# Kernel tuning notes

Measured on AMD Instinct MI355X. Metric: run time of the kernel, lower is better.

The kernel has to match this reference:

```python
import jax, jax.numpy as jnp
import numpy as np
import math

NUM_HEADS = 16
HEAD_SIZE = 64
SEQ_LEN = 2048
D_MODEL = NUM_HEADS * HEAD_SIZE
BATCH = 2


def _xavier(key, shape):
    fan_in, fan_out = shape[0], shape[1]
    limit = math.sqrt(6.0 / (fan_in + fan_out))
    return jax.random.uniform(key, shape, jnp.float32, -limit, limit)


def setup_inputs() -> dict:
    key = jax.random.key(0)
    ks = jax.random.split(key, 5)
    x = jax.random.normal(ks[0], (BATCH, SEQ_LEN, D_MODEL), jnp.float32)
    W_Q = _xavier(ks[1], (D_MODEL, D_MODEL))
    W_K = _xavier(ks[2], (D_MODEL, D_MODEL))
    W_V = _xavier(ks[3], (D_MODEL, D_MODEL))
    W_O = _xavier(ks[4], (D_MODEL, D_MODEL))
    zeros = jnp.zeros((D_MODEL,), jnp.float32)
    return {
        "x": x,
        "W_Q": W_Q, "W_K": W_K, "W_V": W_V, "W_O": W_O,
        "b_Q": zeros, "b_K": zeros, "b_V": zeros, "b_O": zeros,
    }


def _split_heads(t):
    # [B, S, H*d] -> [B, H, S, d]
    B, S, _ = t.shape
    return t.reshape(B, S, NUM_HEADS, HEAD_SIZE).transpose(0, 2, 1, 3)


def reference(x, W_Q, W_K, W_V, W_O, b_Q, b_K, b_V, b_O):
    q = _split_heads(x @ W_Q + b_Q)  # [B,H,S,d]
    k = _split_heads(x @ W_K + b_K)
    v = _split_heads(x @ W_V + b_V)

    # scores: [B,H,S,S]
    scores = jnp.einsum("bhqd,bhkd->bhqk", q, k)
    # Faithful to original: multiply by lower-triangular 0/1 mask, scale,
    # then add -10000 on strictly-upper positions (NOT -inf).
    tril = jnp.tril(jnp.ones((SEQ_LEN, SEQ_LEN), jnp.float32))
    neg_bias = jnp.triu(jnp.full((SEQ_LEN, SEQ_LEN), -10000.0, jnp.float32), 1)
    masked = scores * tril / np.sqrt(HEAD_SIZE).astype(np.float32) + neg_bias
    weights = jax.nn.softmax(masked, axis=-1)

    hs = jnp.einsum("bhqk,bhkd->bhqd", weights, v)  # [B,H,S,d]
    B = hs.shape[0]
    merged = hs.transpose(0, 2, 1, 3).reshape(B, SEQ_LEN, D_MODEL)
    return merged @ W_O + b_O
```

## Files before the change

### kernel.cpp

```cpp
#include <hip/hip_runtime.h>
#include <hip/hip_bf16.h>

#define S_LEN 2048
#define NH 16
#define HD 64
#define DM 1024
#define BATCH 2
#define M_ROWS (BATCH * S_LEN)
#define SCALE2 0.18033688011112043f
#define M2FIX 8.0f

typedef float f32x4 __attribute__((ext_vector_type(4)));
typedef __bf16 bf16x8 __attribute__((ext_vector_type(8)));
typedef short short8 __attribute__((ext_vector_type(8)));

__device__ __forceinline__ unsigned short f2bf(float f) {
  unsigned u = __builtin_bit_cast(unsigned, f);
  u += 0x7FFFu + ((u >> 16) & 1u);
  return (unsigned short)(u >> 16);
}

__device__ __forceinline__ f32x4 mfma16(bf16x8 a, bf16x8 b, f32x4 c) {
  return __builtin_amdgcn_mfma_f32_16x16x32_bf16(a, b, c, 0, 0, 0);
}

__device__ __forceinline__ void gload_lds16(const void* g, void* l) {
  __builtin_amdgcn_global_load_lds(
      (const __attribute__((address_space(1))) void*)g,
      (__attribute__((address_space(3))) void*)l, 16, 0, 0);
}

__global__ __launch_bounds__(256) void cast_bf16_kernel(
    const float* __restrict__ in, unsigned short* __restrict__ out) {
  int i = blockIdx.x * 256 + threadIdx.x;
  const float4* p = (const float4*)in;
  float4 f0 = p[i * 2], f1 = p[i * 2 + 1];
  short8 o;
  o[0] = (short)f2bf(f0.x); o[1] = (short)f2bf(f0.y);
  o[2] = (short)f2bf(f0.z); o[3] = (short)f2bf(f0.w);
  o[4] = (short)f2bf(f1.x); o[5] = (short)f2bf(f1.y);
  o[6] = (short)f2bf(f1.z); o[7] = (short)f2bf(f1.w);
  ((short8*)out)[i] = o;
}

__global__ __launch_bounds__(256) void transpose_cast_kernel(
    const float* __restrict__ W0, const float* __restrict__ W1,
    const float* __restrict__ W2, const float* __restrict__ W3,
    unsigned short* __restrict__ out) {
  int z = blockIdx.z;
  const float* W = (z == 0) ? W0 : (z == 1) ? W1 : (z == 2) ? W2 : W3;
  __shared__ float tile[32][33];
  int tx = threadIdx.x & 31, ty = threadIdx.x >> 5;
  int bx = blockIdx.x * 32, by = blockIdx.y * 32;
#pragma unroll
  for (int i = 0; i < 4; ++i)
    tile[ty + i * 8][tx] = W[(size_t)(by + ty + i * 8) * DM + bx + tx];
  __syncthreads();
  unsigned short* o = out + (size_t)z * DM * DM;
#pragma unroll
  for (int i = 0; i < 4; ++i)
    o[(size_t)(bx + ty + i * 8) * DM + by + tx] = f2bf(tile[tx][ty + i * 8]);
}

template <int MODE>
__global__ __launch_bounds__(256) void gemm_bt_kernel(
    const unsigned short* __restrict__ A, const unsigned short* __restrict__ Bt,
    void* __restrict__ Cptr, const float* __restrict__ bias0,
    const float* __restrict__ bias1, const float* __restrict__ bias2,
    int M, int N, int K) {
  __shared__ __align__(16) unsigned short Sbuf[2][3][4096];
  unsigned short (*As)[4096] = Sbuf[0];
  unsigned short (*Bs)[4096] = Sbuf[1];
  const int t = threadIdx.x, lane = t & 63;
  const int wid = t >> 6, wr = wid >> 1, wc = wid & 1;
  const int r16 = lane & 15, g = lane >> 4;
  const int m0 = blockIdx.y * 128, n0 = blockIdx.x * 128;
  const int nk = K >> 5;

  const int n1 = t, n2 = t + 256;
  const int r1g = t >> 2, c1g = (t & 3) * 8;
  const int r2g = (t + 256) >> 2;

  const unsigned short* ap1 = A + (size_t)(m0 + r1g) * K + c1g;
  const unsigned short* ap2 = A + (size_t)(m0 + r2g) * K + c1g;
  const unsigned short* bp1 = Bt + (size_t)(n0 + r1g) * K + c1g;
  const unsigned short* bp2 = Bt + (size_t)(n0 + r2g) * K + c1g;

#define GSTAGE(s)                          \
  gload_lds16(ap1, &As[s][n1 * 8]);        \
  gload_lds16(bp1, &Bs[s][n1 * 8]);        \
  gload_lds16(ap2, &As[s][n2 * 8]);        \
  gload_lds16(bp2, &Bs[s][n2 * 8]);        \
  ap1 += 32; ap2 += 32; bp1 += 32; bp2 += 32;

  f32x4 acc[4][4] = {};

  GSTAGE(0);
  GSTAGE(1);

  for (int kt = 0; kt < nk; ++kt) {
    const int cs = kt % 3;
    if (kt + 1 < nk) {
      asm volatile("s_waitcnt vmcnt(4)" ::: "memory");
    } else {
      asm volatile("s_waitcnt vmcnt(0)" ::: "memory");
    }
    __builtin_amdgcn_s_barrier();
    if (kt + 2 < nk) { GSTAGE((kt + 2) % 3); }

    bf16x8 af[4], bfr[4];
#pragma unroll
    for (int mi = 0; mi < 4; ++mi)
      af[mi] = *(const bf16x8*)&As[cs][(wr * 64 + mi * 16 + r16) * 32 + g * 8];
#pragma unroll
    for (int ni = 0; ni < 4; ++ni)
      bfr[ni] = *(const bf16x8*)&Bs[cs][(wc * 64 + ni * 16 + r16) * 32 + g * 8];
    __builtin_amdgcn_s_setprio(1);
#pragma unroll
    for (int mi = 0; mi < 4; ++mi)
#pragma unroll
      for (int ni = 0; ni < 4; ++ni)
        acc[mi][ni] = mfma16(af[mi], bfr[ni], acc[mi][ni]);
    __builtin_amdgcn_s_setprio(0);
  }
#undef GSTAGE

  if (MODE == 0) {
    unsigned short* Cb = (unsigned short*)Cptr;
    const int buf = n0 >> 10;
    if (buf < 2) {
      const float* bp = buf ? bias1 : bias0;
      const float sc = buf ? 1.0f : SCALE2;
#pragma unroll
      for (int ni = 0; ni < 4; ++ni) {
        int cn = (n0 & 1023) + wc * 64 + ni * 16 + r16;
        float bv = bp[cn];
#pragma unroll
        for (int mi = 0; mi < 4; ++mi) {
          int rowb = m0 + wr * 64 + mi * 16 + 4 * g;
#pragma unroll
          for (int j = 0; j < 4; ++j)
            Cb[(size_t)buf * 4194304u + (size_t)(rowb + j) * 1024 + cn] =
                __builtin_bit_cast(unsigned short, (__bf16)((acc[mi][ni][j] + bv) * sc));
        }
      }
    } else {
      unsigned short* T = &Sbuf[0][0][0];
      __syncthreads();
#pragma unroll
      for (int ni = 0; ni < 4; ++ni) {
        int cnl = wc * 64 + ni * 16 + r16;
        float bv = bias2[(n0 & 1023) + cnl];
#pragma unroll
        for (int mi = 0; mi < 4; ++mi) {
          int sl = wr * 64 + mi * 16 + 4 * g;
          union { __bf16 h4[4]; uint2 u; } cv;
#pragma unroll
          for (int j = 0; j < 4; ++j) cv.h4[j] = (__bf16)(acc[mi][ni][j] + bv);
          *(uint2*)&T[cnl * 136 + sl] = cv.u;
        }
      }
      __syncthreads();
      const int bb = m0 >> 11, s0g = m0 & 2047;
      unsigned short* Vt = Cb + 8388608u;
#pragma unroll
      for (int p = 0; p < 8; ++p) {
        int idx = p * 256 + t;
        int cnl = idx >> 4, sch = idx & 15;
        int cng = (n0 & 1023) + cnl;
        int hh = cng >> 6, d = cng & 63;
        short8 v = *(const short8*)&T[cnl * 136 + sch * 8];
        *(short8*)&Vt[(((size_t)((bb * 16 + hh) * 64 + d)) << 11) + s0g + sch * 8] = v;
      }
    }
  } else {
    float* Cf = (float*)Cptr;
#pragma unroll
    for (int ni = 0; ni < 4; ++ni) {
      int col = n0 + wc * 64 + ni * 16 + r16;
      float bv = bias0[col];
#pragma unroll
      for (int mi = 0; mi < 4; ++mi) {
        int rowb = m0 + wr * 64 + mi * 16 + 4 * g;
#pragma unroll
        for (int j = 0; j < 4; ++j)
          Cf[(size_t)(rowb + j) * N + col] = acc[mi][ni][j] + bv;
      }
    }
  }
}

__global__ __launch_bounds__(256) void attn_kernel(
    const unsigned short* __restrict__ Qm, const unsigned short* __restrict__ Km,
    const unsigned short* __restrict__ VtG, unsigned short* __restrict__ Om) {
  const int t = threadIdx.x, lane = t & 63, w = t >> 6;
  const int r16 = lane & 15, g = lane >> 4;
  const int bid = blockIdx.x;
  const int xk = bid & 7, slot = bid >> 3;
  const int grp = xk + 8 * (slot >> 4);
  const int mq = slot & 15;
  const int h = grp & 15, b = grp >> 4;

  __shared__ __align__(16) unsigned short Ks[2][8192];
  __shared__ __align__(16) unsigned short Vs[2][8192];
  __shared__ __align__(16) unsigned short Pl[4608];

  const unsigned short* Kbase = Km + (size_t)(b * S_LEN) * DM + h * HD;
  const unsigned short* Vbase = VtG + (size_t)((b * NH + h) * HD) * S_LEN;

  const int kc = ((t & 7) ^ ((t >> 3) & 7)) * 8;
  const int vc = ((t & 15) ^ (t >> 4)) * 8;
  const unsigned short* kp = Kbase + (size_t)(t >> 3) * DM + kc;
  const unsigned short* vp = Vbase + (size_t)(t >> 4) * S_LEN + vc;
  const int sxk = r16 & 7;
  const int qloc = w * 16 + r16;

  unsigned short* Pw = &Pl[w * 1152];
  unsigned* Pw32 = (unsigned*)Pw;

#define STAGE(s, kv0)                                                          \
  do {                                                                         \
    _Pragma("unroll") for (int p = 0; p < 4; ++p)                              \
        gload_lds16(kp + (size_t)((kv0) + 32 * p) * DM, &Ks[s][(t + 256 * p) * 8]); \
    _Pragma("unroll") for (int p = 0; p < 4; ++p)                              \
        gload_lds16(vp + (size_t)(16 * p) * S_LEN + (kv0), &Vs[s][(t + 256 * p) * 8]); \
  } while (0)

  for (int half = 0; half < 2; ++half) {
    const int qt = half ? 31 - mq : mq;
    const int q0 = qt * 64;
    const unsigned short* Qp = Qm + (size_t)(b * S_LEN + q0 + qloc) * DM + h * HD;
    bf16x8 qf0 = *(const bf16x8*)(Qp + g * 8);
    bf16x8 qf1 = *(const bf16x8*)(Qp + 32 + g * 8);

    f32x4 oacc[4] = {};
    float lsum = 0.f;
    const int nt2 = (qt + 2) >> 1;

    __syncthreads();
    STAGE(0, 0);

    for (int kt = 0; kt < nt2; ++kt) {
      const int cs = kt & 1;
      asm volatile("s_waitcnt vmcnt(0)" ::: "memory");
      __builtin_amdgcn_s_barrier();
      if (kt + 1 < nt2) { STAGE(cs ^ 1, (kt + 1) * 128); }

      const int kvbase = kt * 128;
#pragma unroll
      for (int u = 0; u < 2; ++u) {
        const int kvs = kvbase + u * 64;
        if (kvs > q0 + 63) break;

        f32x4 st[4];
#pragma unroll
        for (int ni = 0; ni < 4; ++ni) {
          int row = u * 64 + ni * 16 + r16;
          f32x4 z = {};
          bf16x8 kf0 = *(const bf16x8*)&Ks[cs][row * 64 + ((g ^ sxk) * 8)];
          bf16x8 kf1 = *(const bf16x8*)&Ks[cs][row * 64 + (((4 + g) ^ sxk) * 8)];
          __builtin_amdgcn_s_setprio(1);
          st[ni] = mfma16(kf1, qf1, mfma16(kf0, qf0, z));
          __builtin_amdgcn_s_setprio(0);
        }

        float p[4][4];
#pragma unroll
        for (int ni = 0; ni < 4; ++ni)
#pragma unroll
          for (int j = 0; j < 4; ++j)
            p[ni][j] = __builtin_amdgcn_exp2f(st[ni][j] - M2FIX);
        if (kvs == q0) {
#pragma unroll
          for (int ni = 0; ni < 4; ++ni)
#pragma unroll
            for (int j = 0; j < 4; ++j) {
              int kvl = ni * 16 + 4 * g + j;
              if (kvl > qloc) p[ni][j] = 0.f;
            }
        }
        lsum += ((p[0][0] + p[0][1]) + (p[0][2] + p[0][3])) +
                ((p[1][0] + p[1][1]) + (p[1][2] + p[1][3])) +
                ((p[2][0] + p[2][1]) + (p[2][2] + p[2][3])) +
                ((p[3][0] + p[3][1]) + (p[3][2] + p[3][3]));

#pragma unroll
        for (int ni = 0; ni < 4; ++ni) {
          union { __bf16 hh[4]; uint2 u2; } cv;
          cv.hh[0] = (__bf16)p[ni][0];
          cv.hh[1] = (__bf16)p[ni][1];
          cv.hh[2] = (__bf16)p[ni][2];
          cv.hh[3] = (__bf16)p[ni][3];
          *(uint2*)&Pw32[r16 * 36 + ni * 8 + 2 * g] = cv.u2;
        }
        bf16x8 pf0 = *(const bf16x8*)&Pw[r16 * 72 + g * 8];
        bf16x8 pf1 = *(const bf16x8*)&Pw[r16 * 72 + 32 + g * 8];

        __builtin_amdgcn_s_setprio(1);
#pragma unroll
        for (int di = 0; di < 4; ++di) {
          int row = di * 16 + r16;
          bf16x8 vf0 = *(const bf16x8*)&Vs[cs][row * 128 + (((u * 8 + g) ^ r16) * 8)];
          bf16x8 vf1 = *(const bf16x8*)&Vs[cs][row * 128 + (((u * 8 + 4 + g) ^ r16) * 8)];
          oacc[di] = mfma16(vf0, pf0, oacc[di]);
          oacc[di] = mfma16(vf1, pf1, oacc[di]);
        }
        __builtin_amdgcn_s_setprio(0);
      }
    }

    lsum += __shfl_xor(lsum, 16);
    lsum += __shfl_xor(lsum, 32);
    float li = 1.0f / lsum;
    unsigned short* op = Om + (size_t)(b * S_LEN + q0 + qloc) * DM + h * HD;
#pragma unroll
    for (int di = 0; di < 4; ++di) {
      union { __bf16 hh[4]; uint2 u2; } ov;
      ov.hh[0] = (__bf16)(oacc[di][0] * li);
      ov.hh[1] = (__bf16)(oacc[di][1] * li);
      ov.hh[2] = (__bf16)(oacc[di][2] * li);
      ov.hh[3] = (__bf16)(oacc[di][3] * li);
      *(uint2*)(op + di * 16 + 4 * g) = ov.u2;
    }
  }
#undef STAGE
}

extern "C" void kernel_launch(void* const* d_in, const int* in_sizes, int n_in,
                              void* d_out, int out_size, void* d_ws, size_t ws_size,
                              hipStream_t stream) {
  (void)in_sizes; (void)n_in; (void)out_size; (void)ws_size;
  const float* x  = (const float*)d_in[0];
  const float* WQ = (const float*)d_in[1];
  const float* WK = (const float*)d_in[2];
  const float* WV = (const float*)d_in[3];
  const float* WO = (const float*)d_in[4];
  const float* bQ = (const float*)d_in[5];
  const float* bK = (const float*)d_in[6];
  const float* bV = (const float*)d_in[7];
  const float* bO = (const float*)d_in[8];

  char* ws = (char*)d_ws;
  unsigned short* xb  = (unsigned short*)(ws);
  unsigned short* wt  = (unsigned short*)(ws + (8u << 20));
  unsigned short* qb  = (unsigned short*)(ws + (16u << 20));
  unsigned short* hsb = (unsigned short*)(ws + (40u << 20));

  cast_bf16_kernel<<<2048, 256, 0, stream>>>(x, xb);
  transpose_cast_kernel<<<dim3(32, 32, 4), 256, 0, stream>>>(WQ, WK, WV, WO, wt);
  gemm_bt_kernel<0><<<dim3(24, 32), 256, 0, stream>>>(
      xb, wt, (void*)qb, bQ, bK, bV, M_ROWS, 3072, DM);
  attn_kernel<<<512, 256, 0, stream>>>(qb, qb + 4194304u, qb + 8388608u, hsb);
  gemm_bt_kernel<1><<<dim3(8, 32), 256, 0, stream>>>(
      hsb, wt + 3u * 1048576u, d_out, bO, nullptr, nullptr, M_ROWS, DM, DM);
}
```

Measured before the change: 105.6 us.

## Make attention waves independent, reading K/V directly from global memory

Drops the block-shared double-buffered LDS staging of K and V tiles along with its barriers. Each wave now owns a 16-row query group and walks only its own causal range of 64-wide KV tiles, loading K and V fragments straight from global/L2. The row sum is computed with an MFMA against a ones vector instead of scalar adds and cross-lane shuffles. This removes synchronisation and per-wave causal imbalance, but gives up K/V reuse across the four waves, so global/L2 traffic and load latency exposure increase.

```diff
diff --git a/kernel.cpp b/kernel.cpp
--- a/kernel.cpp
+++ b/kernel.cpp
@@ -194,125 +194,99 @@
     const unsigned short* __restrict__ Qm, const unsigned short* __restrict__ Km,
     const unsigned short* __restrict__ VtG, unsigned short* __restrict__ Om) {
   const int t = threadIdx.x, lane = t & 63, w = t >> 6;
-  const int r16 = lane & 15, g = lane >> 4;
+  const int r16 = lane & 15, fg = lane >> 4;
   const int bid = blockIdx.x;
   const int xk = bid & 7, slot = bid >> 3;
-  const int grp = xk + 8 * (slot >> 4);
-  const int mq = slot & 15;
+  const int grp = xk * 4 + (slot >> 4);
   const int h = grp & 15, b = grp >> 4;
-
-  __shared__ __align__(16) unsigned short Ks[2][8192];
-  __shared__ __align__(16) unsigned short Vs[2][8192];
-  __shared__ __align__(16) unsigned short Pl[4608];
-
-  const unsigned short* Kbase = Km + (size_t)(b * S_LEN) * DM + h * HD;
-  const unsigned short* Vbase = VtG + (size_t)((b * NH + h) * HD) * S_LEN;
-
-  const int kc = ((t & 7) ^ ((t >> 3) & 7)) * 8;
-  const int vc = ((t & 15) ^ (t >> 4)) * 8;
-  const unsigned short* kp = Kbase + (size_t)(t >> 3) * DM + kc;
-  const unsigned short* vp = Vbase + (size_t)(t >> 4) * S_LEN + vc;
-  const int sxk = r16 & 7;
-  const int qloc = w * 16 + r16;
-
-  unsigned short* Pw = &Pl[w * 1152];
+  const int pair = (slot & 15) * 4 + w;
+
+  __shared__ __align__(16) unsigned short Pl[4][1152];
+  unsigned short* Pw = Pl[w];
   unsigned* Pw32 = (unsigned*)Pw;
 
-#define STAGE(s, kv0)                                                          \
-  do {                                                                         \
-    _Pragma("unroll") for (int p = 0; p < 4; ++p)                              \
-        gload_lds16(kp + (size_t)((kv0) + 32 * p) * DM, &Ks[s][(t + 256 * p) * 8]); \
-    _Pragma("unroll") for (int p = 0; p < 4; ++p)                              \
-        gload_lds16(vp + (size_t)(16 * p) * S_LEN + (kv0), &Vs[s][(t + 256 * p) * 8]); \
-  } while (0)
+  const unsigned short* Kb = Km + (size_t)(b * S_LEN) * DM + h * HD;
+  const unsigned short* Vb = VtG + (size_t)((b * NH + h) * HD) * S_LEN;
+
+  bf16x8 ones;
+#pragma unroll
+  for (int e = 0; e < 8; ++e) ones[e] = (__bf16)1.0f;
 
   for (int half = 0; half < 2; ++half) {
-    const int qt = half ? 31 - mq : mq;
-    const int q0 = qt * 64;
-    const unsigned short* Qp = Qm + (size_t)(b * S_LEN + q0 + qloc) * DM + h * HD;
-    bf16x8 qf0 = *(const bf16x8*)(Qp + g * 8);
-    bf16x8 qf1 = *(const bf16x8*)(Qp + 32 + g * 8);
+    const int qg = half ? 127 - pair : pair;
+    const int qrow = qg * 16 + r16;
+    const int ntk = (qg >> 2) + 1;
+    const int diag = qg >> 2;
+    const int qrel = ((qg & 3) << 4) + r16;
+
+    const unsigned short* Qp = Qm + (size_t)(b * S_LEN + qrow) * DM + h * HD;
+    bf16x8 qf0 = *(const bf16x8*)(Qp + fg * 8);
+    bf16x8 qf1 = *(const bf16x8*)(Qp + 32 + fg * 8);
 
     f32x4 oacc[4] = {};
-    float lsum = 0.f;
-    const int nt2 = (qt + 2) >> 1;
-
-    __syncthreads();
-    STAGE(0, 0);
-
-    for (int kt = 0; kt < nt2; ++kt) {
-      const int cs = kt & 1;
-      asm volatile("s_waitcnt vmcnt(0)" ::: "memory");
-      __builtin_amdgcn_s_barrier();
-      if (kt + 1 < nt2) { STAGE(cs ^ 1, (kt + 1) * 128); }
-
-      const int kvbase = kt * 128;
-#pragma unroll
-      for (int u = 0; u < 2; ++u) {
-        const int kvs = kvbase + u * 64;
-        if (kvs > q0 + 63) break;
-
-        f32x4 st[4];
-#pragma unroll
-        for (int ni = 0; ni < 4; ++ni) {
-          int row = u * 64 + ni * 16 + r16;
-          f32x4 z = {};
-          bf16x8 kf0 = *(const bf16x8*)&Ks[cs][row * 64 + ((g ^ sxk) * 8)];
-          bf16x8 kf1 = *(const bf16x8*)&Ks[cs][row * 64 + (((4 + g) ^ sxk) * 8)];
-          __builtin_amdgcn_s_setprio(1);
-          st[ni] = mfma16(kf1, qf1, mfma16(kf0, qf0, z));
-          __builtin_amdgcn_s_setprio(0);
-        }
-
-        float p[4][4];
+    f32x4 lacc = {};
+
+    for (int kt = 0; kt < ntk; ++kt) {
+      const int kv0 = kt * 64;
+      const unsigned short* Kt = Kb + (size_t)kv0 * DM;
+      const unsigned short* Vt0 = Vb + kv0;
+
+      f32x4 st[4];
+#pragma unroll
+      for (int ni = 0; ni < 4; ++ni) {
+        const unsigned short* kr = Kt + (size_t)(ni * 16 + r16) * DM;
+        bf16x8 kf0 = *(const bf16x8*)(kr + fg * 8);
+        bf16x8 kf1 = *(const bf16x8*)(kr + 32 + fg * 8);
+        f32x4 z = {};
+        __builtin_amdgcn_s_setprio(1);
+        st[ni] = mfma16(kf1, qf1, mfma16(kf0, qf0, z));
+        __builtin_amdgcn_s_setprio(0);
+      }
+
+      float p[4][4];
+#pragma unroll
+      for (int ni = 0; ni < 4; ++ni)
+#pragma unroll
+        for (int j = 0; j < 4; ++j)
+          p[ni][j] = __builtin_amdgcn_exp2f(st[ni][j] - M2FIX);
+      if (kt == diag) {
 #pragma unroll
         for (int ni = 0; ni < 4; ++ni)
 #pragma unroll
-          for (int j = 0; j < 4; ++j)
-            p[ni][j] = __builtin_amdgcn_exp2f(st[ni][j] - M2FIX);
-        if (kvs == q0) {
-#pragma unroll
-          for (int ni = 0; ni < 4; ++ni)
-#pragma unroll
-            for (int j = 0; j < 4; ++j) {
-              int kvl = ni * 16 + 4 * g + j;
-              if (kvl > qloc) p[ni][j] = 0.f;
-            }
-        }
-        lsum += ((p[0][0] + p[0][1]) + (p[0][2] + p[0][3])) +
-                ((p[1][0] + p[1][1]) + (p[1][2] + p[1][3])) +
-                ((p[2][0] + p[2][1]) + (p[2][2] + p[2][3])) +
-                ((p[3][0] + p[3][1]) + (p[3][2] + p[3][3]));
-
-#pragma unroll
-        for (int ni = 0; ni < 4; ++ni) {
-          union { __bf16 hh[4]; uint2 u2; } cv;
-          cv.hh[0] = (__bf16)p[ni][0];
-          cv.hh[1] = (__bf16)p[ni][1];
-          cv.hh[2] = (__bf16)p[ni][2];
-          cv.hh[3] = (__bf16)p[ni][3];
-          *(uint2*)&Pw32[r16 * 36 + ni * 8 + 2 * g] = cv.u2;
-        }
-        bf16x8 pf0 = *(const bf16x8*)&Pw[r16 * 72 + g * 8];
-        bf16x8 pf1 = *(const bf16x8*)&Pw[r16 * 72 + 32 + g * 8];
-
-        __builtin_amdgcn_s_setprio(1);
-#pragma unroll
-        for (int di = 0; di < 4; ++di) {
-          int row = di * 16 + r16;
-          bf16x8 vf0 = *(const bf16x8*)&Vs[cs][row * 128 + (((u * 8 + g) ^ r16) * 8)];
-          bf16x8 vf1 = *(const bf16x8*)&Vs[cs][row * 128 + (((u * 8 + 4 + g) ^ r16) * 8)];
-          oacc[di] = mfma16(vf0, pf0, oacc[di]);
-          oacc[di] = mfma16(vf1, pf1, oacc[di]);
-        }
-        __builtin_amdgcn_s_setprio(0);
-      }
-    }
-
-    lsum += __shfl_xor(lsum, 16);
-    lsum += __shfl_xor(lsum, 32);
-    float li = 1.0f / lsum;
-    unsigned short* op = Om + (size_t)(b * S_LEN + q0 + qloc) * DM + h * HD;
+          for (int j = 0; j < 4; ++j) {
+            int kvl = ni * 16 + 4 * fg + j;
+            if (kvl > qrel) p[ni][j] = 0.f;
+          }
+      }
+
+#pragma unroll
+      for (int ni = 0; ni < 4; ++ni) {
+        union { __bf16 hh[4]; uint2 u2; } cv;
+        cv.hh[0] = (__bf16)p[ni][0];
+        cv.hh[1] = (__bf16)p[ni][1];
+        cv.hh[2] = (__bf16)p[ni][2];
+        cv.hh[3] = (__bf16)p[ni][3];
+        *(uint2*)&Pw32[r16 * 36 + ni * 8 + 2 * fg] = cv.u2;
+      }
+      bf16x8 pf0 = *(const bf16x8*)&Pw[r16 * 72 + fg * 8];
+      bf16x8 pf1 = *(const bf16x8*)&Pw[r16 * 72 + 32 + fg * 8];
+
+      lacc = mfma16(ones, pf1, mfma16(ones, pf0, lacc));
+
+      __builtin_amdgcn_s_setprio(1);
+#pragma unroll
+      for (int di = 0; di < 4; ++di) {
+        const unsigned short* vr = Vt0 + (size_t)(di * 16 + r16) * S_LEN;
+        bf16x8 vf0 = *(const bf16x8*)(vr + fg * 8);
+        bf16x8 vf1 = *(const bf16x8*)(vr + 32 + fg * 8);
+        oacc[di] = mfma16(vf0, pf0, oacc[di]);
+        oacc[di] = mfma16(vf1, pf1, oacc[di]);
+      }
+      __builtin_amdgcn_s_setprio(0);
+    }
+
+    float li = 1.0f / lacc[0];
+    unsigned short* op = Om + (size_t)(b * S_LEN + qrow) * DM + h * HD;
 #pragma unroll
     for (int di = 0; di < 4; ++di) {
       union { __bf16 hh[4]; uint2 u2; } ov;
@@ -320,10 +294,9 @@
       ov.hh[1] = (__bf16)(oacc[di][1] * li);
       ov.hh[2] = (__bf16)(oacc[di][2] * li);
       ov.hh[3] = (__bf16)(oacc[di][3] * li);
-      *(uint2*)(op + di * 16 + 4 * g) = ov.u2;
+      *(uint2*)(op + di * 16 + 4 * fg) = ov.u2;
     }
   }
-#undef STAGE
 }
 
 extern "C" void kernel_launch(void* const* d_in, const int* in_sizes, int n_in,
```

After: 185.5 us. 1.76x slower.
